# Kernel tuning notes

Hardware: AMD Instinct MI355X
Metric: run time of the kernel (lower is better)

Reference implementation:

```python
import jax, jax.numpy as jnp
import numpy as np

RATIO = 0.6
ROT_FACTOR = 0.1  # fraction of 2*pi
B, H, W, C = 32, 512, 512, 3
S = 2 * max(H, W)  # mask side = 2*max(H, W) = 1024
FILL_VALUE = 1  # source references undefined self.fill_value; stripes are set to 1


def setup_inputs() -> dict:
    key = jax.random.key(0)
    k1, k2 = jax.random.split(key)
    images = jax.random.uniform(k1, (B, H, W, C), jnp.float32) * 255.0
    max_ang = ROT_FACTOR * 2.0 * np.pi
    angles = jax.random.uniform(k2, (B,), jnp.float32, -max_ang, max_ang)
    rng = np.random.default_rng(0)
    lo = int(min(H * 0.5, W * 0.3))
    hi = int(max(H * 0.5, W * 0.3))
    gridblock = rng.integers(lo, hi + 1, size=B).astype(np.int32)
    start1 = rng.integers(0, gridblock + 1).astype(np.int32)  # uniform [0, gridblock]
    start2 = rng.integers(0, gridblock + 1).astype(np.int32)
    return {
        "images": images,
        "angles": angles,
        "gridblock": jnp.asarray(gridblock),
        "start1": jnp.asarray(start1),
        "start2": jnp.asarray(start2),
    }


def _build_masks(gridblock, start1, start2):
    # Vectorized equivalent of the nested scatter loops: mask[i,j] = 1 iff
    # row i is in a stripe (pass 1) OR column j is in a stripe (pass 2).
    gb = gridblock[:, None].astype(jnp.int32)  # [B,1]
    length = jnp.clip((gb.astype(jnp.float32) * RATIO + 0.5).astype(jnp.int32), 1, gb - 1)
    n = S // gb  # number of stripes per image
    r = jnp.arange(S, dtype=jnp.int32)[None, :]  # [1,S]

    def stripes(start):
        d = r - start[:, None]
        return (d >= 0) & (jnp.mod(d, gb) < length) & ((d // gb) < n)

    rows = stripes(start1)  # [B,S]
    cols = stripes(start2)  # [B,S]
    return (rows[:, :, None] | cols[:, None, :]).astype(jnp.float32)  # [B,S,S]


def _rotate_bilinear_reflect(mask, angles):
    # Rotate each mask about its center by angles[b] (CCW), bilinear interp,
    # reflect fill (TF 'reflect': d c b a | a b c d | d c b a).
    c = (S - 1) / 2.0
    yy, xx = jnp.meshgrid(jnp.arange(S, dtype=jnp.float32),
                          jnp.arange(S, dtype=jnp.float32), indexing="ij")
    cos = jnp.cos(angles)[:, None, None]
    sin = jnp.sin(angles)[:, None, None]
    x = xx[None] - c
    y = yy[None] - c
    sx = cos * x + sin * y + c  # inverse-map source coords [B,S,S]
    sy = -sin * x + cos * y + c
    x0 = jnp.floor(sx)
    y0 = jnp.floor(sy)
    fx = sx - x0
    fy = sy - y0
    x0i = x0.astype(jnp.int32)
    y0i = y0.astype(jnp.int32)

    def refl(i):
        m = jnp.mod(i, 2 * S)
        return jnp.where(m < S, m, 2 * S - 1 - m)

    x0r, x1r = refl(x0i), refl(x0i + 1)
    y0r, y1r = refl(y0i), refl(y0i + 1)
    b = jnp.arange(mask.shape[0])[:, None, None]
    v00 = mask[b, y0r, x0r]
    v01 = mask[b, y0r, x1r]
    v10 = mask[b, y1r, x0r]
    v11 = mask[b, y1r, x1r]
    return (v00 * (1 - fx) * (1 - fy) + v01 * fx * (1 - fy)
            + v10 * (1 - fx) * fy + v11 * fx * fy)


def reference(images, angles, gridblock, start1, start2):
    mask = _build_masks(gridblock, start1, start2) * FILL_VALUE  # [B,S,S]
    rot = _rotate_bilinear_reflect(mask, angles)
    off_h = (S - H) // 2
    off_w = (S - W) // 2
    m = rot[:, off_h:off_h + H, off_w:off_w + W]  # center crop [B,H,W]
    return images * m[..., None]
```

## Files before the change

kernel.cpp:

```cpp
#include <hip/hip_runtime.h>

namespace {
constexpr int S = 1024;
constexpr int H = 512;
constexpr int W = 512;
constexpr int B = 32;
constexpr int OFF = 256;

__device__ __forceinline__ int refl(int i) {
    int m = i & (2 * S - 1);
    return (m < S) ? m : (2 * S - 1 - m);
}

__device__ __forceinline__ bool stripe(int i, int start, int gb, int len, int n, float inv_gb) {
    int d = i - start;
    if (d < 0) return false;
    int q = (int)((float)d * inv_gb);
    int r = d - q * gb;
    if (r < 0)        { r += gb; --q; }
    else if (r >= gb) { r -= gb; ++q; }
    return (r < len) && (q < n);
}

__global__ __launch_bounds__(256) void gridmask_kernel(
    const float* __restrict__ images,
    const float* __restrict__ angles,
    const int* __restrict__ gridblock,
    const int* __restrict__ start1,
    const int* __restrict__ start2,
    float* __restrict__ out)
{
    __shared__ float mlds[1024];

    const int tid = threadIdx.x;
    const int blk = blockIdx.x;
    const int b   = blk >> 8;
    const int pix_base = (blk & 255) << 10;

    {
        const int p0   = tid << 2;
        const int gpix = pix_base + p0;
        const int y    = gpix >> 9;
        const int x    = gpix & 511;

        const float ang = angles[b];
        const int gb = gridblock[b];
        const int s1 = start1[b];
        const int s2 = start2[b];

        const float gbf = (float)gb;
        int len = (int)(__fadd_rn(__fmul_rn(gbf, 0.6f), 0.5f));
        len = min(max(len, 1), gb - 1);
        const int n = S / gb;
        const float inv_gb = 1.0f / gbf;

        float sn, cs;
        sincosf(ang, &sn, &cs);

        const float c = (float)(S - 1) * 0.5f;
        const float Y = (float)(y + OFF) - c;

        float m[4];
#pragma unroll
        for (int i = 0; i < 4; ++i) {
            const float X  = (float)(x + i + OFF) - c;
            const float sx =  cs * X + sn * Y + c;
            const float sy =  cs * Y - sn * X + c;
            const float x0f = floorf(sx);
            const float y0f = floorf(sy);
            const float fx = sx - x0f;
            const float fy = sy - y0f;
            const int x0i = (int)x0f;
            const int y0i = (int)y0f;
            const int x0r = refl(x0i), x1r = refl(x0i + 1);
            const int y0r = refl(y0i), y1r = refl(y0i + 1);
            const bool c0 = stripe(x0r, s2, gb, len, n, inv_gb);
            const bool c1 = stripe(x1r, s2, gb, len, n, inv_gb);
            const bool r0 = stripe(y0r, s1, gb, len, n, inv_gb);
            const bool r1 = stripe(y1r, s1, gb, len, n, inv_gb);
            const float v00 = (r0 | c0) ? 1.0f : 0.0f;
            const float v01 = (r0 | c1) ? 1.0f : 0.0f;
            const float v10 = (r1 | c0) ? 1.0f : 0.0f;
            const float v11 = (r1 | c1) ? 1.0f : 0.0f;
            m[i] = (v00 * (1.0f - fx) + v01 * fx) * (1.0f - fy)
                 + (v10 * (1.0f - fx) + v11 * fx) * fy;
        }
        float4* ml4 = (float4*)mlds;
        ml4[tid] = make_float4(m[0], m[1], m[2], m[3]);
    }
    __syncthreads();

    const size_t fbase = (size_t)blk * 3072;
    const float4* __restrict__ gin4  = (const float4*)(images + fbase);
    float4* __restrict__       gout4 = (float4*)(out + fbase);

    const float4 p0 = gin4[tid];
    const float4 p1 = gin4[tid + 256];
    const float4 p2 = gin4[tid + 512];

#pragma unroll
    for (int j = 0; j < 3; ++j) {
        const int lf = (j << 10) + (tid << 2);
        const int q  = lf / 3;
        const int r  = lf - q * 3;
        const float ma = mlds[q];
        const float mb = mlds[q + 1 <= 1023 ? q + 1 : 1023];
        const float m0 = (r + 0 >= 3) ? mb : ma;
        const float m1 = (r + 1 >= 3) ? mb : ma;
        const float m2 = (r + 2 >= 3) ? mb : ma;
        const float m3 = (r + 3 >= 3) ? mb : ma;
        const float4 p = (j == 0) ? p0 : (j == 1) ? p1 : p2;
        float4 o;
        o.x = p.x * m0;
        o.y = p.y * m1;
        o.z = p.z * m2;
        o.w = p.w * m3;
        gout4[(j << 8) + tid] = o;
    }
}
}

extern "C" void kernel_launch(void* const* d_in, const int* in_sizes, int n_in,
                              void* d_out, int out_size, void* d_ws, size_t ws_size,
                              hipStream_t stream) {
    const float* images    = (const float*)d_in[0];
    const float* angles    = (const float*)d_in[1];
    const int*   gridblock = (const int*)d_in[2];
    const int*   start1    = (const int*)d_in[3];
    const int*   start2    = (const int*)d_in[4];
    float* outp = (float*)d_out;

    const int blocks = B * H * W / 1024;
    gridmask_kernel<<<blocks, 256, 0, stream>>>(images, angles, gridblock, start1, start2, outp);
}
```

Measured before the change: 182.2 us.

## Precompute per-image stripe tables and factor bilinear mask as separable OR

Each block now handles 8 image rows and first builds per-image row and column stripe tables in LDS, each entry holding a value and its forward difference. Interpolating along each axis and combining with cx+ry-cx*ry matches the bilinear blend of the OR mask for 0/1 stripes. This removes four integer-divide-style stripe tests and the reflect step per output pixel, replacing them with two LDS lookups and a few FMAs. It also loads the image data before the mask computation, doubles the block size and uses nontemporal stores. Dropping the reflect step assumes rotated coordinates always stay inside the mask, which holds for this fixed crop and angle range.

```diff
diff --git a/kernel.cpp b/kernel.cpp
--- a/kernel.cpp
+++ b/kernel.cpp
@@ -2,27 +2,21 @@
 
 namespace {
 constexpr int S = 1024;
-constexpr int H = 512;
-constexpr int W = 512;
 constexpr int B = 32;
 constexpr int OFF = 256;
 
-__device__ __forceinline__ int refl(int i) {
-    int m = i & (2 * S - 1);
-    return (m < S) ? m : (2 * S - 1 - m);
-}
+typedef float f32x4 __attribute__((ext_vector_type(4)));
 
-__device__ __forceinline__ bool stripe(int i, int start, int gb, int len, int n, float inv_gb) {
-    int d = i - start;
-    if (d < 0) return false;
+__device__ __forceinline__ float stripef(int i, int start, int gb, int len, int n, float inv_gb) {
+    const int d = i - start;
     int q = (int)((float)d * inv_gb);
     int r = d - q * gb;
     if (r < 0)        { r += gb; --q; }
     else if (r >= gb) { r -= gb; ++q; }
-    return (r < len) && (q < n);
+    return (d >= 0 && r < len && q < n) ? 1.0f : 0.0f;
 }
 
-__global__ __launch_bounds__(256) void gridmask_kernel(
+__global__ __launch_bounds__(512) void gridmask_kernel(
     const float* __restrict__ images,
     const float* __restrict__ angles,
     const int* __restrict__ gridblock,
@@ -30,92 +24,90 @@
     const int* __restrict__ start2,
     float* __restrict__ out)
 {
-    __shared__ float mlds[1024];
+    __shared__ float2 colsAD[1024];
+    __shared__ float2 rowsAD[1024];
+    __shared__ float  mlds[4096];
 
     const int tid = threadIdx.x;
     const int blk = blockIdx.x;
-    const int b   = blk >> 8;
-    const int pix_base = (blk & 255) << 10;
+    const int b   = blk >> 6;
+    const int y0  = (blk & 63) << 3;
+
+    const size_t fbase = (size_t)blk * 12288;
+    const float4* __restrict__ gin4 = (const float4*)(images + fbase);
+    float4 p[6];
+#pragma unroll
+    for (int j = 0; j < 6; ++j) p[j] = gin4[(j << 9) + tid];
+
+    const float ang = angles[b];
+    const int gb = gridblock[b];
+    const int s1 = start1[b];
+    const int s2 = start2[b];
+
+    const float gbf = (float)gb;
+    int len = (int)(__fadd_rn(__fmul_rn(gbf, 0.6f), 0.5f));
+    len = min(max(len, 1), gb - 1);
+    const int n = S / gb;
+    const float inv_gb = 1.0f / gbf;
 
     {
-        const int p0   = tid << 2;
-        const int gpix = pix_base + p0;
-        const int y    = gpix >> 9;
-        const int x    = gpix & 511;
+        const int i0 = tid << 1;
+        const float r0 = stripef(i0,     s1, gb, len, n, inv_gb);
+        const float r1 = stripef(i0 + 1, s1, gb, len, n, inv_gb);
+        const float r2 = stripef(i0 + 2, s1, gb, len, n, inv_gb);
+        rowsAD[i0]     = make_float2(r0, r1 - r0);
+        rowsAD[i0 + 1] = make_float2(r1, r2 - r1);
+        const float c0 = stripef(i0,     s2, gb, len, n, inv_gb);
+        const float c1 = stripef(i0 + 1, s2, gb, len, n, inv_gb);
+        const float c2 = stripef(i0 + 2, s2, gb, len, n, inv_gb);
+        colsAD[i0]     = make_float2(c0, c1 - c0);
+        colsAD[i0 + 1] = make_float2(c1, c2 - c1);
+    }
+    __syncthreads();
 
-        const float ang = angles[b];
-        const int gb = gridblock[b];
-        const int s1 = start1[b];
-        const int s2 = start2[b];
-
-        const float gbf = (float)gb;
-        int len = (int)(__fadd_rn(__fmul_rn(gbf, 0.6f), 0.5f));
-        len = min(max(len, 1), gb - 1);
-        const int n = S / gb;
-        const float inv_gb = 1.0f / gbf;
-
+    {
         float sn, cs;
         sincosf(ang, &sn, &cs);
-
         const float c = (float)(S - 1) * 0.5f;
-        const float Y = (float)(y + OFF) - c;
-
-        float m[4];
+        const float X = (float)(tid + OFF) - c;
 #pragma unroll
-        for (int i = 0; i < 4; ++i) {
-            const float X  = (float)(x + i + OFF) - c;
-            const float sx =  cs * X + sn * Y + c;
-            const float sy =  cs * Y - sn * X + c;
+        for (int r = 0; r < 8; ++r) {
+            const float Yr = (float)(y0 + r + OFF) - c;
+            const float sx = cs * X + sn * Yr + c;
+            const float sy = cs * Yr - sn * X + c;
             const float x0f = floorf(sx);
             const float y0f = floorf(sy);
             const float fx = sx - x0f;
             const float fy = sy - y0f;
-            const int x0i = (int)x0f;
-            const int y0i = (int)y0f;
-            const int x0r = refl(x0i), x1r = refl(x0i + 1);
-            const int y0r = refl(y0i), y1r = refl(y0i + 1);
-            const bool c0 = stripe(x0r, s2, gb, len, n, inv_gb);
-            const bool c1 = stripe(x1r, s2, gb, len, n, inv_gb);
-            const bool r0 = stripe(y0r, s1, gb, len, n, inv_gb);
-            const bool r1 = stripe(y1r, s1, gb, len, n, inv_gb);
-            const float v00 = (r0 | c0) ? 1.0f : 0.0f;
-            const float v01 = (r0 | c1) ? 1.0f : 0.0f;
-            const float v10 = (r1 | c0) ? 1.0f : 0.0f;
-            const float v11 = (r1 | c1) ? 1.0f : 0.0f;
-            m[i] = (v00 * (1.0f - fx) + v01 * fx) * (1.0f - fy)
-                 + (v10 * (1.0f - fx) + v11 * fx) * fy;
+            const int xi = (int)x0f;
+            const int yi = (int)y0f;
+            const float2 cad = colsAD[xi];
+            const float2 rad = rowsAD[yi];
+            const float cx = fmaf(fx, cad.y, cad.x);
+            const float ry = fmaf(fy, rad.y, rad.x);
+            mlds[(r << 9) + tid] = cx + ry - cx * ry;
         }
-        float4* ml4 = (float4*)mlds;
-        ml4[tid] = make_float4(m[0], m[1], m[2], m[3]);
     }
     __syncthreads();
 
-    const size_t fbase = (size_t)blk * 3072;
-    const float4* __restrict__ gin4  = (const float4*)(images + fbase);
-    float4* __restrict__       gout4 = (float4*)(out + fbase);
-
-    const float4 p0 = gin4[tid];
-    const float4 p1 = gin4[tid + 256];
-    const float4 p2 = gin4[tid + 512];
-
+    f32x4* __restrict__ gout4 = (f32x4*)(out + fbase);
 #pragma unroll
-    for (int j = 0; j < 3; ++j) {
-        const int lf = (j << 10) + (tid << 2);
+    for (int j = 0; j < 6; ++j) {
+        const int lf = (j << 11) + (tid << 2);
         const int q  = lf / 3;
         const int r  = lf - q * 3;
         const float ma = mlds[q];
-        const float mb = mlds[q + 1 <= 1023 ? q + 1 : 1023];
-        const float m0 = (r + 0 >= 3) ? mb : ma;
+        const float mb = mlds[min(q + 1, 4095)];
+        const float m0 = ma;
         const float m1 = (r + 1 >= 3) ? mb : ma;
         const float m2 = (r + 2 >= 3) ? mb : ma;
         const float m3 = (r + 3 >= 3) ? mb : ma;
-        const float4 p = (j == 0) ? p0 : (j == 1) ? p1 : p2;
-        float4 o;
-        o.x = p.x * m0;
-        o.y = p.y * m1;
-        o.z = p.z * m2;
-        o.w = p.w * m3;
-        gout4[(j << 8) + tid] = o;
+        f32x4 o;
+        o.x = p[j].x * m0;
+        o.y = p[j].y * m1;
+        o.z = p[j].z * m2;
+        o.w = p[j].w * m3;
+        __builtin_nontemporal_store(o, gout4 + (j << 9) + tid);
     }
 }
 }
@@ -130,6 +122,5 @@
     const int*   start2    = (const int*)d_in[4];
     float* outp = (float*)d_out;
 
-    const int blocks = B * H * W / 1024;
-    gridmask_kernel<<<blocks, 256, 0, stream>>>(images, angles, gridblock, start1, start2, outp);
+    gridmask_kernel<<<2048, 512, 0, stream>>>(images, angles, gridblock, start1, start2, outp);
 }
```

Measured after the change: 183.1 us. No clear change (+0.5%).
